# Kernel tuning notes

Measured on AMD Instinct MI355X. Metric: run time of the kernel, lower is better.

The kernel has to match this reference:

```python
import jax, jax.numpy as jnp
import numpy as np

N_NODES = 50000
N_EDGES = 1600000
HID = 128
REST = 96  # (hidden//4) x 1e vectors = 32*3
N_MP = 2


def _linear_init(key, fan_in, fan_out):
    return jax.random.normal(key, (fan_in, fan_out), dtype=jnp.float32) / np.sqrt(fan_in)


def setup_inputs() -> dict:
    key = jax.random.key(0)
    ks = jax.random.split(key, 16)
    h = jax.random.normal(ks[0], (N_NODES, HID + REST), dtype=jnp.float32)
    edge_index = jax.random.randint(ks[1], (2, N_EDGES), 0, N_NODES, dtype=jnp.int32)
    edge_len = jax.random.uniform(ks[2], (N_EDGES,), dtype=jnp.float32) * 5.0
    # ScalarMessagePassing MLPs: Linear(2*HID+1 -> HID), SiLU, Linear(HID -> HID), stacked per layer
    mp_w1 = jnp.stack([_linear_init(ks[3 + i], 2 * HID + 1, HID) for i in range(N_MP)])
    mp_b1 = jnp.zeros((N_MP, HID), dtype=jnp.float32)
    mp_w2 = jnp.stack([_linear_init(ks[5 + i], HID, HID) for i in range(N_MP)])
    mp_b2 = jnp.zeros((N_MP, HID), dtype=jnp.float32)
    # NodeUpdateMLP: Linear(HID -> HID), SiLU, Linear(HID -> HID)
    nu_w1 = _linear_init(ks[7], HID, HID)
    nu_b1 = jnp.zeros((HID,), dtype=jnp.float32)
    nu_w2 = _linear_init(ks[8], HID, HID)
    nu_b2 = jnp.zeros((HID,), dtype=jnp.float32)
    return dict(h=h, edge_index=edge_index, edge_len=edge_len,
                mp_w1=mp_w1, mp_b1=mp_b1, mp_w2=mp_w2, mp_b2=mp_b2,
                nu_w1=nu_w1, nu_b1=nu_b1, nu_w2=nu_w2, nu_b2=nu_b2)


def _scalar_mp(scalars, sender, receiver, edge_len, w1, b1, w2, b2):
    # gather -> MLP -> index_add scatter, residual on scalar channels
    msg_in = jnp.concatenate([scalars[sender], scalars[receiver], edge_len[:, None]], axis=-1)  # [E, 2H+1]
    msgs = jax.nn.silu(msg_in @ w1 + b1) @ w2 + b2  # [E, H]
    agg = jax.ops.segment_sum(msgs, receiver, num_segments=scalars.shape[0])  # [N, H]
    return scalars + agg


def reference(h, edge_index, edge_len, mp_w1, mp_b1, mp_w2, mp_b2, nu_w1, nu_b1, nu_w2, nu_b2):
    scalars, rest = h[..., :HID], h[..., HID:]
    sender, receiver = edge_index[0], edge_index[1]
    for i in range(N_MP):
        scalars = _scalar_mp(scalars, sender, receiver, edge_len,
                             mp_w1[i], mp_b1[i], mp_w2[i], mp_b2[i])
    # NodeUpdateMLP: scalars + MLP(scalars)
    scalars = scalars + (jax.nn.silu(scalars @ nu_w1 + nu_b1) @ nu_w2 + nu_b2)
    return jnp.concatenate([scalars, rest], axis=-1)
```

## Files before the change

### kernel.cpp

```cpp
#include <hip/hip_runtime.h>
#include <hip/hip_fp16.h>


#define NFEAT 224
#define RBITS 8
#define NB 196
#define CAP 10240

typedef _Float16 v8h __attribute__((ext_vector_type(8)));
typedef float f32x4 __attribute__((ext_vector_type(4)));

#define MFMA16(a, b, c) __builtin_amdgcn_mfma_f32_16x16x32_f16(a, b, c, 0, 0, 0)

__device__ __forceinline__ float silu_f(float x) {
    float e = __expf(-x);
    return x * __builtin_amdgcn_rcpf(1.0f + e);
}

__global__ void k_prep(const float* __restrict__ mp_w1, const float* __restrict__ mp_w2,
                       const float* __restrict__ nu_w1, const float* __restrict__ nu_w2,
                       _Float16* __restrict__ Wp,
                       const float4* __restrict__ h4, float4* __restrict__ out4, int N) {
    if (blockIdx.x < 8) {
        const float* srcs[8] = {
            mp_w1, mp_w1 + 16384, mp_w2,
            mp_w1 + 32896, mp_w1 + 32896 + 16384, mp_w2 + 16384,
            nu_w1, nu_w2
        };
        const float* W = srcs[blockIdx.x];
        _Float16* dst = Wp + (size_t)blockIdx.x * 16384;
        for (int i = 0; i < 8; ++i) {
            int u = threadIdx.x + i * 256;
            int nt = u >> 8;
            int kt = (u >> 6) & 3;
            int lane = u & 63;
            int kb = kt * 32 + (lane >> 4) * 8;
            int n = nt * 16 + (lane & 15);
#pragma unroll
            for (int j = 0; j < 8; ++j)
                dst[(size_t)u * 8 + j] = (_Float16)W[(size_t)(kb + j) * 128 + n];
        }
    } else {
        int b = blockIdx.x - 8;
        int t = threadIdx.x;
        if (t < 240) {
            int r = b * 10 + t / 24;
            int c = t % 24;
            if (r < N) out4[(size_t)r * 56 + 32 + c] = h4[(size_t)r * 56 + 32 + c];
        }
    }
}

__global__ void cs_bucket(const int* __restrict__ recv, const int* __restrict__ sender,
                          const float* __restrict__ elen, int* __restrict__ cnt,
                          int* __restrict__ br, unsigned* __restrict__ bsl,
                          int E, int chunk) {
    __shared__ int lhist[256];
    __shared__ int lcur[256];
    int t = threadIdx.x;
    int start = blockIdx.x * chunk;
    int end = start + chunk; if (end > E) end = E;
    lhist[t] = 0;
    __syncthreads();
    for (int i = start + t; i < end; i += 256)
        atomicAdd(&lhist[recv[i] >> RBITS], 1);
    __syncthreads();
    if (t < NB) {
        int c = lhist[t];
        lcur[t] = t * CAP + (c ? atomicAdd(&cnt[t], c) : 0);
    }
    __syncthreads();
    for (int i = start + t; i < end; i += 256) {
        int r = recv[i];
        int pos = atomicAdd(&lcur[r >> RBITS], 1);
        br[pos] = r;
        bsl[pos] = (unsigned)sender[i] |
                   ((unsigned)__half_as_ushort(__float2half_rn(elen[i])) << 16);
    }
}

__global__ void cs_csr(const int* __restrict__ cnt, const int* __restrict__ br,
                       const unsigned* __restrict__ bsl,
                       int* __restrict__ deg, int* __restrict__ rowstart,
                       unsigned* __restrict__ epack, int N) {
    __shared__ int hist[256];
    __shared__ int sh[256];
    __shared__ int lcur[256];
    int t = threadIdx.x;
    int b = blockIdx.x;
    int r0 = b << RBITS;
    int e0 = b * CAP;
    int e1 = e0 + cnt[b];
    hist[t] = 0;
    __syncthreads();
    for (int i = e0 + t; i < e1; i += 256)
        atomicAdd(&hist[br[i] & 255], 1);
    __syncthreads();
    sh[t] = hist[t];
    __syncthreads();
    for (int off = 1; off < 256; off <<= 1) {
        int add = (t >= off) ? sh[t - off] : 0;
        __syncthreads();
        sh[t] += add;
        __syncthreads();
    }
    int excl = (t == 0) ? 0 : sh[t - 1];
    lcur[t] = e0 + excl;
    int r = r0 + t;
    if (r < N) { deg[r] = hist[t]; rowstart[r] = e0 + excl; }
    __syncthreads();
    for (int i = e0 + t; i < e1; i += 256) {
        int rr = br[i];
        int pos = atomicAdd(&lcur[rr & 255], 1);
        epack[pos] = bsl[i];
    }
}


#define MM_STAGE_A_F32(Aptr, ldA)                                           \
    _Pragma("unroll") for (int i = 0; i < 4; ++i) {                         \
        int u = threadIdx.x + i * 256;                                      \
        int r = u >> 4;                                                     \
        int g = u & 15;                                                     \
        int gr = blockIdx.x * 64 + r;                                       \
        float4 x0 = make_float4(0.f, 0.f, 0.f, 0.f);                        \
        float4 x1 = x0;                                                     \
        if (gr < M) {                                                       \
            const float* s_ = (Aptr) + (size_t)gr * (ldA) + g * 8;          \
            x0 = *(const float4*)s_;                                        \
            x1 = *(const float4*)(s_ + 4);                                  \
        }                                                                   \
        v8h hv;                                                             \
        hv[0] = (_Float16)x0.x; hv[1] = (_Float16)x0.y;                     \
        hv[2] = (_Float16)x0.z; hv[3] = (_Float16)x0.w;                     \
        hv[4] = (_Float16)x1.x; hv[5] = (_Float16)x1.y;                     \
        hv[6] = (_Float16)x1.z; hv[7] = (_Float16)x1.w;                     \
        Af[((r >> 4) * 4 + (g >> 2)) * 64 + (g & 3) * 16 + (r & 15)] = hv;  \
    }

#define MM_STAGE_A_F16(Aptr)                                                \
    _Pragma("unroll") for (int i = 0; i < 4; ++i) {                         \
        int u = threadIdx.x + i * 256;                                      \
        int r = u >> 4;                                                     \
        int g = u & 15;                                                     \
        int gr = blockIdx.x * 64 + r;                                       \
        float4 x = make_float4(0.f, 0.f, 0.f, 0.f);                         \
        if (gr < M) x = *(const float4*)((Aptr) + (size_t)gr * 128 + g * 8);\
        *(float4*)&Af[((r >> 4) * 4 + (g >> 2)) * 64 + (g & 3) * 16 + (r & 15)] = x; \
    }

#define MM_WAVE_PROLOG                                                      \
    __syncthreads();                                                        \
    const int wv = threadIdx.x >> 6;                                        \
    const int lane = threadIdx.x & 63;                                      \
    const int q_ = lane >> 4;                                               \
    const int c0_ = lane & 15;                                              \
    v8h a0 = Af[(wv * 4 + 0) * 64 + lane];                                  \
    v8h a1 = Af[(wv * 4 + 1) * 64 + lane];                                  \
    v8h a2 = Af[(wv * 4 + 2) * 64 + lane];                                  \
    v8h a3 = Af[(wv * 4 + 3) * 64 + lane];                                  \
    const int grb = blockIdx.x * 64 + wv * 16 + q_ * 4;

#define MM_COMPUTE_B(WPTR, ...)                                             \
    {                                                                       \
        const v8h* Bp_ = (const v8h*)(WPTR) + lane;                         \
        _Pragma("unroll") for (int nt = 0; nt < 8; ++nt) {                  \
            v8h b0 = Bp_[nt * 256];                                         \
            v8h b1v = Bp_[nt * 256 + 64];                                   \
            v8h b2v = Bp_[nt * 256 + 128];                                  \
            v8h b3v = Bp_[nt * 256 + 192];                                  \
            f32x4 c = {0.f, 0.f, 0.f, 0.f};                                 \
            c = MFMA16(a0, b0, c);                                          \
            c = MFMA16(a1, b1v, c);                                         \
            c = MFMA16(a2, b2v, c);                                         \
            c = MFMA16(a3, b3v, c);                                         \
            const int col = nt * 16 + c0_;                                  \
            __VA_ARGS__                                                     \
        }                                                                   \
    }

__launch_bounds__(256)
__global__ void k_mm_xsrb2(const float* __restrict__ A, int ldA,
                           const _Float16* __restrict__ Wp0, const float* __restrict__ b1,
                           _Float16* __restrict__ Xs, _Float16* __restrict__ Xrb, int M) {
    __shared__ v8h Af[1024];
    MM_STAGE_A_F32(A, ldA)
    MM_WAVE_PROLOG
    MM_COMPUTE_B(Wp0, {
        _Pragma("unroll") for (int i = 0; i < 4; ++i) {
            int gr = grb + i;
            if (gr < M) Xs[(size_t)gr * 128 + col] = (_Float16)c[i];
        }
    })
    MM_COMPUTE_B(Wp0 + 16384, {
        float bc = b1[col];
        _Pragma("unroll") for (int i = 0; i < 4; ++i) {
            int gr = grb + i;
            if (gr < M) Xrb[(size_t)gr * 128 + col] = (_Float16)(c[i] + bc);
        }
    })
}

__launch_bounds__(256)
__global__ void k_mm_acc(const _Float16* __restrict__ A, const _Float16* __restrict__ Wp,
                         const float* __restrict__ b2, const int* __restrict__ deg,
                         const float* __restrict__ Sin, int ldSin,
                         float* __restrict__ Sout, int M) {
    __shared__ v8h Af[1024];
    MM_STAGE_A_F16(A)
    MM_WAVE_PROLOG
    MM_COMPUTE_B(Wp, {
        float bc = b2[col];
        _Pragma("unroll") for (int i = 0; i < 4; ++i) {
            int gr = grb + i;
            if (gr < M) {
                float s = Sin[(size_t)gr * ldSin + col];
                Sout[(size_t)gr * 128 + col] = s + c[i] + bc * (float)deg[gr];
            }
        }
    })
}

__launch_bounds__(256)
__global__ void k_mm_nodeupd(const float* __restrict__ S, const _Float16* __restrict__ Wp1,
                             const float* __restrict__ b1, const _Float16* __restrict__ Wp2,
                             const float* __restrict__ b2, float* __restrict__ out, int M) {
    __shared__ v8h Af[1024];
    __shared__ v8h Af2[1024];
    MM_STAGE_A_F32(S, 128)
    MM_WAVE_PROLOG
    _Float16* A2 = (_Float16*)Af2;
    MM_COMPUTE_B(Wp1, {
        float bc = b1[col];
        int kt = col >> 5;
        int o = col & 31;
        int qp = o >> 3;
        int j = o & 7;
        int base = ((wv * 4 + kt) * 64 + qp * 16 + q_ * 4) * 8 + j;
        _Pragma("unroll") for (int i = 0; i < 4; ++i)
            A2[base + i * 8] = (_Float16)silu_f(c[i] + bc);
    })
    __syncthreads();
    a0 = Af2[(wv * 4 + 0) * 64 + lane];
    a1 = Af2[(wv * 4 + 1) * 64 + lane];
    a2 = Af2[(wv * 4 + 2) * 64 + lane];
    a3 = Af2[(wv * 4 + 3) * 64 + lane];
    MM_COMPUTE_B(Wp2, {
        float bc = b2[col];
        _Pragma("unroll") for (int i = 0; i < 4; ++i) {
            int gr = grb + i;
            if (gr < M)
                out[(size_t)gr * NFEAT + col] = S[(size_t)gr * 128 + col] + c[i] + bc;
        }
    })
}

__launch_bounds__(256)
__global__ void k_edge(const __half2* __restrict__ Xs, const __half2* __restrict__ Xrb,
                       const float* __restrict__ w1L, const unsigned* __restrict__ epack,
                       const int* __restrict__ rowstart, const int* __restrict__ deg,
                       __half2* __restrict__ P, int N) {
    int wid = (blockIdx.x * blockDim.x + threadIdx.x) >> 6;
    int lane = threadIdx.x & 63;
    if (wid >= N) return;
    int lo = __builtin_amdgcn_readfirstlane(rowstart[wid]);
    int dg = __builtin_amdgcn_readfirstlane(deg[wid]);
    const unsigned* ep = epack + lo;
    __half2 xr = Xrb[(size_t)wid * 64 + lane];
    float2 wlf = *(const float2*)(w1L + lane * 2);
    __half2 wl = __floats2half2_rn(wlf.x, wlf.y);
    const __half2 one2 = __floats2half2_rn(1.f, 1.f);
    const __half2 nl2e = __floats2half2_rn(-1.44269504f, -1.44269504f);
    float ax = 0.f, ay = 0.f;
    int k = 0;
    unsigned pc[8];
    if (k + 8 <= dg) {
#pragma unroll
        for (int u = 0; u < 8; ++u) pc[u] = ep[u];
    }
    for (; k + 8 <= dg; ) {
        int kn = k + 8;
        unsigned pn[8];
        if (kn + 8 <= dg) {
#pragma unroll
            for (int u = 0; u < 8; ++u) pn[u] = ep[kn + u];
        }
        __half2 x[8];
#pragma unroll
        for (int u = 0; u < 8; ++u)
            x[u] = Xs[(size_t)(pc[u] & 0xFFFFu) * 64 + lane];
        __half2 t2 = __floats2half2_rn(0.f, 0.f);
#pragma unroll
        for (int u = 0; u < 8; ++u) {
            __half2 l2 = __half2half2(__ushort_as_half((unsigned short)(pc[u] >> 16)));
            __half2 pre = __hfma2(l2, wl, __hadd2(x[u], xr));
            __half2 e = h2exp2(__hmul2(pre, nl2e));
            __half2 sil = __hmul2(pre, h2rcp(__hadd2(e, one2)));
            t2 = __hadd2(t2, sil);
        }
        float2 tf = __half22float2(t2);
        ax += tf.x; ay += tf.y;
        k = kn;
#pragma unroll
        for (int u = 0; u < 8; ++u) pc[u] = pn[u];
    }
    for (; k < dg; ++k) {
        unsigned p = ep[k];
        __half2 l2 = __half2half2(__ushort_as_half((unsigned short)(p >> 16)));
        __half2 x = Xs[(size_t)(p & 0xFFFFu) * 64 + lane];
        __half2 pre = __hfma2(l2, wl, __hadd2(x, xr));
        __half2 e = h2exp2(__hmul2(pre, nl2e));
        __half2 sil = __hmul2(pre, h2rcp(__hadd2(e, one2)));
        float2 sf = __half22float2(sil);
        ax += sf.x; ay += sf.y;
    }
    P[(size_t)wid * 64 + lane] = __floats2half2_rn(ax, ay);
}

extern "C" void kernel_launch(void* const* d_in, const int* in_sizes, int n_in,
                              void* d_out, int out_size, void* d_ws, size_t ws_size,
                              hipStream_t stream) {
    const float* h      = (const float*)d_in[0];
    const int*   eidx   = (const int*)d_in[1];
    const float* elen   = (const float*)d_in[2];
    const float* mp_w1  = (const float*)d_in[3];
    const float* mp_b1  = (const float*)d_in[4];
    const float* mp_w2  = (const float*)d_in[5];
    const float* mp_b2  = (const float*)d_in[6];
    const float* nu_w1  = (const float*)d_in[7];
    const float* nu_b1  = (const float*)d_in[8];
    const float* nu_w2  = (const float*)d_in[9];
    const float* nu_b2  = (const float*)d_in[10];
    float* out = (float*)d_out;

    const int N = in_sizes[0] / NFEAT;
    const int E = in_sizes[2];
    const int* sender   = eidx;
    const int* receiver = eidx + E;

    char* w = (char*)d_ws;
    auto alloc = [&](size_t bytes) -> char* {
        char* p = w;
        w += (bytes + 255) & ~(size_t)255;
        return p;
    };
    float*    S     = (float*)alloc((size_t)N * 128 * 4);
    _Float16* Pf    = (_Float16*)alloc((size_t)N * 128 * 2);
    _Float16* Xs16  = (_Float16*)alloc((size_t)N * 128 * 2);
    _Float16* Xrb16 = (_Float16*)alloc((size_t)N * 128 * 2);
    _Float16* Wp    = (_Float16*)alloc((size_t)8 * 16384 * 2);
    int*      br    = (int*)alloc((size_t)NB * CAP * 4);
    unsigned* bsl   = (unsigned*)alloc((size_t)NB * CAP * 4);
    unsigned* epack = (unsigned*)alloc((size_t)NB * CAP * 4);
    int*      deg      = (int*)alloc((size_t)N * 4);
    int*      rowstart = (int*)alloc((size_t)N * 4);
    int*      cnt      = (int*)alloc((size_t)NB * 4);

    (void)hipMemsetAsync(cnt, 0, (size_t)NB * 4, stream);
    k_prep<<<8 + (N + 9) / 10, 256, 0, stream>>>(mp_w1, mp_w2, nu_w1, nu_w2, Wp,
                                                 (const float4*)h, (float4*)out, N);
    const int chunk = 4096;
    cs_bucket<<<(E + chunk - 1) / chunk, 256, 0, stream>>>(receiver, sender, elen, cnt,
                                                           br, bsl, E, chunk);
    cs_csr<<<NB, 256, 0, stream>>>(cnt, br, bsl, deg, rowstart, epack, N);

    const int gb = (N + 63) / 64;
    const int eb = (N * 64 + 255) / 256;

    for (int l = 0; l < 2; ++l) {
        const float* b1 = mp_b1 + (size_t)l * 128;
        const float* b2 = mp_b2 + (size_t)l * 128;
        const float* w1L = mp_w1 + (size_t)l * 32896 + 32768;
        const float* Ain = l ? S : h;
        const int    ldA = l ? 128 : NFEAT;
        k_mm_xsrb2<<<gb, 256, 0, stream>>>(Ain, ldA, Wp + (size_t)(l * 3) * 16384,
                                           b1, Xs16, Xrb16, N);
        k_edge<<<eb, 256, 0, stream>>>((const __half2*)Xs16, (const __half2*)Xrb16,
                                       w1L, epack, rowstart, deg, (__half2*)Pf, N);
        k_mm_acc<<<gb, 256, 0, stream>>>(Pf, Wp + (size_t)(l * 3 + 2) * 16384, b2, deg,
                                         Ain, ldA, S, N);
    }
    k_mm_nodeupd<<<gb, 256, 0, stream>>>(S, Wp + (size_t)6 * 16384, nu_b1,
                                         Wp + (size_t)7 * 16384, nu_b2, out, N);
}
```

Measured before the change: 410.5 us.

## Fuse node matmuls across layers and use rational SiLU in edge kernel

Fuses each layer's W2 accumulation with the next stage's matmuls: acc feeds directly into the layer-2 Xs/Xrb projection, and the final acc is fused with the node-update MLP, keeping the updated scalars in LDS and registers rather than re-reading them from memory. The edge kernel now prefetches the next batch of gathered Xs rows while computing the current batch, and replaces the exp-based SiLU with a clamped rational tanh approximation in packed fp16. This removes two launches and some global round-trips, and shortens the per-edge math. In exchange the approximation slightly changes SiLU accuracy, and register use rises.

```diff
diff --git a/kernel.cpp b/kernel.cpp
--- a/kernel.cpp
+++ b/kernel.cpp
@@ -8,6 +8,7 @@
 #define CAP 10240
 
 typedef _Float16 v8h __attribute__((ext_vector_type(8)));
+typedef _Float16 v2h __attribute__((ext_vector_type(2)));
 typedef float f32x4 __attribute__((ext_vector_type(4)));
 
 #define MFMA16(a, b, c) __builtin_amdgcn_mfma_f32_16x16x32_f16(a, b, c, 0, 0, 0)
@@ -161,6 +162,12 @@
     v8h a3 = Af[(wv * 4 + 3) * 64 + lane];                                  \
     const int grb = blockIdx.x * 64 + wv * 16 + q_ * 4;
 
+#define MM_RELOAD_A(SRC)                                                    \
+    a0 = SRC[(wv * 4 + 0) * 64 + lane];                                     \
+    a1 = SRC[(wv * 4 + 1) * 64 + lane];                                     \
+    a2 = SRC[(wv * 4 + 2) * 64 + lane];                                     \
+    a3 = SRC[(wv * 4 + 3) * 64 + lane];
+
 #define MM_COMPUTE_B(WPTR, ...)                                             \
     {                                                                       \
         const v8h* Bp_ = (const v8h*)(WPTR) + lane;                         \
@@ -179,6 +186,13 @@
         }                                                                   \
     }
 
+#define MM_EXCHANGE_IDX                                                     \
+    int kt = col >> 5;                                                      \
+    int o = col & 31;                                                       \
+    int qp = o >> 3;                                                        \
+    int j = o & 7;                                                          \
+    int base = ((wv * 4 + kt) * 64 + qp * 16 + q_ * 4) * 8 + j;
+
 __launch_bounds__(256)
 __global__ void k_mm_xsrb2(const float* __restrict__ A, int ldA,
                            const _Float16* __restrict__ Wp0, const float* __restrict__ b1,
@@ -202,119 +216,171 @@
 }
 
 __launch_bounds__(256)
-__global__ void k_mm_acc(const _Float16* __restrict__ A, const _Float16* __restrict__ Wp,
-                         const float* __restrict__ b2, const int* __restrict__ deg,
-                         const float* __restrict__ Sin, int ldSin,
-                         float* __restrict__ Sout, int M) {
-    __shared__ v8h Af[1024];
-    MM_STAGE_A_F16(A)
-    MM_WAVE_PROLOG
-    MM_COMPUTE_B(Wp, {
-        float bc = b2[col];
-        _Pragma("unroll") for (int i = 0; i < 4; ++i) {
-            int gr = grb + i;
-            if (gr < M) {
-                float s = Sin[(size_t)gr * ldSin + col];
-                Sout[(size_t)gr * 128 + col] = s + c[i] + bc * (float)deg[gr];
-            }
-        }
-    })
-}
-
-__launch_bounds__(256)
-__global__ void k_mm_nodeupd(const float* __restrict__ S, const _Float16* __restrict__ Wp1,
-                             const float* __restrict__ b1, const _Float16* __restrict__ Wp2,
-                             const float* __restrict__ b2, float* __restrict__ out, int M) {
+__global__ void k_mm_accxsrb(const _Float16* __restrict__ P, const _Float16* __restrict__ Ww2,
+                             const float* __restrict__ b2, const int* __restrict__ deg,
+                             const float* __restrict__ Sin, int ldSin,
+                             float* __restrict__ Sout,
+                             const _Float16* __restrict__ Wp1, const float* __restrict__ b1,
+                             _Float16* __restrict__ Xs, _Float16* __restrict__ Xrb, int M) {
     __shared__ v8h Af[1024];
     __shared__ v8h Af2[1024];
-    MM_STAGE_A_F32(S, 128)
+    MM_STAGE_A_F16(P)
     MM_WAVE_PROLOG
     _Float16* A2 = (_Float16*)Af2;
+    MM_COMPUTE_B(Ww2, {
+        float bc = b2[col];
+        MM_EXCHANGE_IDX
+        _Pragma("unroll") for (int i = 0; i < 4; ++i) {
+            int gr = grb + i;
+            float sv = 0.f;
+            if (gr < M) {
+                sv = Sin[(size_t)gr * ldSin + col] + c[i] + bc * (float)deg[gr];
+                Sout[(size_t)gr * 128 + col] = sv;
+            }
+            A2[base + i * 8] = (_Float16)sv;
+        }
+    })
+    __syncthreads();
+    MM_RELOAD_A(Af2)
     MM_COMPUTE_B(Wp1, {
+        _Pragma("unroll") for (int i = 0; i < 4; ++i) {
+            int gr = grb + i;
+            if (gr < M) Xs[(size_t)gr * 128 + col] = (_Float16)c[i];
+        }
+    })
+    MM_COMPUTE_B(Wp1 + 16384, {
         float bc = b1[col];
-        int kt = col >> 5;
-        int o = col & 31;
-        int qp = o >> 3;
-        int j = o & 7;
-        int base = ((wv * 4 + kt) * 64 + qp * 16 + q_ * 4) * 8 + j;
+        _Pragma("unroll") for (int i = 0; i < 4; ++i) {
+            int gr = grb + i;
+            if (gr < M) Xrb[(size_t)gr * 128 + col] = (_Float16)(c[i] + bc);
+        }
+    })
+}
+
+__launch_bounds__(256)
+__global__ void k_mm_accnode(const _Float16* __restrict__ P, const _Float16* __restrict__ Ww2,
+                             const float* __restrict__ b2, const int* __restrict__ deg,
+                             const float* __restrict__ Sin,
+                             const _Float16* __restrict__ Wn1, const float* __restrict__ nb1,
+                             const _Float16* __restrict__ Wn2, const float* __restrict__ nb2,
+                             float* __restrict__ out, int M) {
+    __shared__ v8h Af[1024];
+    __shared__ v8h Af2[1024];
+    MM_STAGE_A_F16(P)
+    MM_WAVE_PROLOG
+    float s2v[8][4];
+    _Float16* A2 = (_Float16*)Af2;
+    MM_COMPUTE_B(Ww2, {
+        float bc = b2[col];
+        MM_EXCHANGE_IDX
+        _Pragma("unroll") for (int i = 0; i < 4; ++i) {
+            int gr = grb + i;
+            float sv = 0.f;
+            if (gr < M) sv = Sin[(size_t)gr * 128 + col] + c[i] + bc * (float)deg[gr];
+            s2v[nt][i] = sv;
+            A2[base + i * 8] = (_Float16)sv;
+        }
+    })
+    __syncthreads();
+    MM_RELOAD_A(Af2)
+    _Float16* A3 = (_Float16*)Af;
+    MM_COMPUTE_B(Wn1, {
+        float bc = nb1[col];
+        MM_EXCHANGE_IDX
         _Pragma("unroll") for (int i = 0; i < 4; ++i)
-            A2[base + i * 8] = (_Float16)silu_f(c[i] + bc);
-    })
-    __syncthreads();
-    a0 = Af2[(wv * 4 + 0) * 64 + lane];
-    a1 = Af2[(wv * 4 + 1) * 64 + lane];
-    a2 = Af2[(wv * 4 + 2) * 64 + lane];
-    a3 = Af2[(wv * 4 + 3) * 64 + lane];
-    MM_COMPUTE_B(Wp2, {
-        float bc = b2[col];
+            A3[base + i * 8] = (_Float16)silu_f(c[i] + bc);
+    })
+    __syncthreads();
+    MM_RELOAD_A(Af)
+    MM_COMPUTE_B(Wn2, {
+        float bc = nb2[col];
         _Pragma("unroll") for (int i = 0; i < 4; ++i) {
             int gr = grb + i;
             if (gr < M)
-                out[(size_t)gr * NFEAT + col] = S[(size_t)gr * 128 + col] + c[i] + bc;
-        }
-    })
+                out[(size_t)gr * NFEAT + col] = s2v[nt][i] + c[i] + bc;
+        }
+    })
+}
+
+__device__ __forceinline__ v2h silu2_pk(v2h pre) {
+    const v2h h27 = {(_Float16)27.f, (_Float16)27.f};
+    const v2h hp3 = {(_Float16)3.f, (_Float16)3.f};
+    const v2h hn3 = {(_Float16)-3.f, (_Float16)-3.f};
+    v2h h = pre * (_Float16)0.5f;
+    v2h z = __builtin_elementwise_min(__builtin_elementwise_max(h, hn3), hp3);
+    v2h z2 = z * z;
+    v2h num = z * (z2 + h27);
+    v2h den = z2 * (_Float16)9.f + h27;
+    __half2 rd = h2rcp(__builtin_bit_cast(__half2, den));
+    v2h u = num * __builtin_bit_cast(v2h, rd);
+    return h * u + h;
 }
 
 __launch_bounds__(256)
-__global__ void k_edge(const __half2* __restrict__ Xs, const __half2* __restrict__ Xrb,
+__global__ void k_edge(const v2h* __restrict__ Xs, const v2h* __restrict__ Xrb,
                        const float* __restrict__ w1L, const unsigned* __restrict__ epack,
                        const int* __restrict__ rowstart, const int* __restrict__ deg,
-                       __half2* __restrict__ P, int N) {
+                       v2h* __restrict__ P, int N) {
     int wid = (blockIdx.x * blockDim.x + threadIdx.x) >> 6;
     int lane = threadIdx.x & 63;
     if (wid >= N) return;
     int lo = __builtin_amdgcn_readfirstlane(rowstart[wid]);
     int dg = __builtin_amdgcn_readfirstlane(deg[wid]);
     const unsigned* ep = epack + lo;
-    __half2 xr = Xrb[(size_t)wid * 64 + lane];
+    v2h xr = Xrb[(size_t)wid * 64 + lane];
     float2 wlf = *(const float2*)(w1L + lane * 2);
-    __half2 wl = __floats2half2_rn(wlf.x, wlf.y);
-    const __half2 one2 = __floats2half2_rn(1.f, 1.f);
-    const __half2 nl2e = __floats2half2_rn(-1.44269504f, -1.44269504f);
+    v2h wl = {(_Float16)wlf.x, (_Float16)wlf.y};
     float ax = 0.f, ay = 0.f;
     int k = 0;
     unsigned pc[8];
+    v2h xc[8];
+    if (dg >= 8) {
+#pragma unroll
+        for (int u = 0; u < 8; ++u) pc[u] = ep[u];
+#pragma unroll
+        for (int u = 0; u < 8; ++u)
+            xc[u] = Xs[(size_t)(pc[u] & 0xFFFFu) * 64 + lane];
+    }
+    for (; k + 16 <= dg; k += 8) {
+        unsigned pn[8];
+        v2h xn[8];
+#pragma unroll
+        for (int u = 0; u < 8; ++u) pn[u] = ep[k + 8 + u];
+#pragma unroll
+        for (int u = 0; u < 8; ++u)
+            xn[u] = Xs[(size_t)(pn[u] & 0xFFFFu) * 64 + lane];
+        v2h t2 = {(_Float16)0.f, (_Float16)0.f};
+#pragma unroll
+        for (int u = 0; u < 8; ++u) {
+            _Float16 lv = __builtin_bit_cast(_Float16, (unsigned short)(pc[u] >> 16));
+            v2h pre = xc[u] + xr + lv * wl;
+            t2 = t2 + silu2_pk(pre);
+        }
+        ax += (float)t2[0]; ay += (float)t2[1];
+#pragma unroll
+        for (int u = 0; u < 8; ++u) { pc[u] = pn[u]; xc[u] = xn[u]; }
+    }
     if (k + 8 <= dg) {
-#pragma unroll
-        for (int u = 0; u < 8; ++u) pc[u] = ep[u];
-    }
-    for (; k + 8 <= dg; ) {
-        int kn = k + 8;
-        unsigned pn[8];
-        if (kn + 8 <= dg) {
-#pragma unroll
-            for (int u = 0; u < 8; ++u) pn[u] = ep[kn + u];
-        }
-        __half2 x[8];
-#pragma unroll
-        for (int u = 0; u < 8; ++u)
-            x[u] = Xs[(size_t)(pc[u] & 0xFFFFu) * 64 + lane];
-        __half2 t2 = __floats2half2_rn(0.f, 0.f);
+        v2h t2 = {(_Float16)0.f, (_Float16)0.f};
 #pragma unroll
         for (int u = 0; u < 8; ++u) {
-            __half2 l2 = __half2half2(__ushort_as_half((unsigned short)(pc[u] >> 16)));
-            __half2 pre = __hfma2(l2, wl, __hadd2(x[u], xr));
-            __half2 e = h2exp2(__hmul2(pre, nl2e));
-            __half2 sil = __hmul2(pre, h2rcp(__hadd2(e, one2)));
-            t2 = __hadd2(t2, sil);
-        }
-        float2 tf = __half22float2(t2);
-        ax += tf.x; ay += tf.y;
-        k = kn;
-#pragma unroll
-        for (int u = 0; u < 8; ++u) pc[u] = pn[u];
+            _Float16 lv = __builtin_bit_cast(_Float16, (unsigned short)(pc[u] >> 16));
+            v2h pre = xc[u] + xr + lv * wl;
+            t2 = t2 + silu2_pk(pre);
+        }
+        ax += (float)t2[0]; ay += (float)t2[1];
+        k += 8;
     }
     for (; k < dg; ++k) {
         unsigned p = ep[k];
-        __half2 l2 = __half2half2(__ushort_as_half((unsigned short)(p >> 16)));
-        __half2 x = Xs[(size_t)(p & 0xFFFFu) * 64 + lane];
-        __half2 pre = __hfma2(l2, wl, __hadd2(x, xr));
-        __half2 e = h2exp2(__hmul2(pre, nl2e));
-        __half2 sil = __hmul2(pre, h2rcp(__hadd2(e, one2)));
-        float2 sf = __half22float2(sil);
-        ax += sf.x; ay += sf.y;
-    }
-    P[(size_t)wid * 64 + lane] = __floats2half2_rn(ax, ay);
+        _Float16 lv = __builtin_bit_cast(_Float16, (unsigned short)(p >> 16));
+        v2h x = Xs[(size_t)(p & 0xFFFFu) * 64 + lane];
+        v2h pre = x + xr + lv * wl;
+        v2h s = silu2_pk(pre);
+        ax += (float)s[0]; ay += (float)s[1];
+    }
+    v2h o = {(_Float16)ax, (_Float16)ay};
+    P[(size_t)wid * 64 + lane] = o;
 }
 
 extern "C" void kernel_launch(void* const* d_in, const int* in_sizes, int n_in,
@@ -344,7 +410,7 @@
         w += (bytes + 255) & ~(size_t)255;
         return p;
     };
-    float*    S     = (float*)alloc((size_t)N * 128 * 4);
+    float*    S1    = (float*)alloc((size_t)N * 128 * 4);
     _Float16* Pf    = (_Float16*)alloc((size_t)N * 128 * 2);
     _Float16* Xs16  = (_Float16*)alloc((size_t)N * 128 * 2);
     _Float16* Xrb16 = (_Float16*)alloc((size_t)N * 128 * 2);
@@ -367,19 +433,19 @@
     const int gb = (N + 63) / 64;
     const int eb = (N * 64 + 255) / 256;
 
-    for (int l = 0; l < 2; ++l) {
-        const float* b1 = mp_b1 + (size_t)l * 128;
-        const float* b2 = mp_b2 + (size_t)l * 128;
-        const float* w1L = mp_w1 + (size_t)l * 32896 + 32768;
-        const float* Ain = l ? S : h;
-        const int    ldA = l ? 128 : NFEAT;
-        k_mm_xsrb2<<<gb, 256, 0, stream>>>(Ain, ldA, Wp + (size_t)(l * 3) * 16384,
-                                           b1, Xs16, Xrb16, N);
-        k_edge<<<eb, 256, 0, stream>>>((const __half2*)Xs16, (const __half2*)Xrb16,
-                                       w1L, epack, rowstart, deg, (__half2*)Pf, N);
-        k_mm_acc<<<gb, 256, 0, stream>>>(Pf, Wp + (size_t)(l * 3 + 2) * 16384, b2, deg,
-                                         Ain, ldA, S, N);
-    }
-    k_mm_nodeupd<<<gb, 256, 0, stream>>>(S, Wp + (size_t)6 * 16384, nu_b1,
-                                         Wp + (size_t)7 * 16384, nu_b2, out, N);
-}
+    k_mm_xsrb2<<<gb, 256, 0, stream>>>(h, NFEAT, Wp, mp_b1, Xs16, Xrb16, N);
+    k_edge<<<eb, 256, 0, stream>>>((const v2h*)Xs16, (const v2h*)Xrb16,
+                                   mp_w1 + 32768, epack, rowstart, deg, (v2h*)Pf, N);
+    k_mm_accxsrb<<<gb, 256, 0, stream>>>(Pf, Wp + (size_t)2 * 16384, mp_b2, deg,
+                                         h, NFEAT, S1,
+                                         Wp + (size_t)3 * 16384, mp_b1 + 128,
+                                         Xs16, Xrb16, N);
+    k_edge<<<eb, 256, 0, stream>>>((const v2h*)Xs16, (const v2h*)Xrb16,
+                                   mp_w1 + 32896 + 32768, epack, rowstart, deg,
+                                   (v2h*)Pf, N);
+    k_mm_accnode<<<gb, 256, 0, stream>>>(Pf, Wp + (size_t)5 * 16384, mp_b2 + 128, deg,
+                                         S1,
+                                         Wp + (size_t)6 * 16384, nu_b1,
+                                         Wp + (size_t)7 * 16384, nu_b2,
+                                         out, N);
+}
```

New measurement: 400.8 us. 1.02x faster.
